# Performance work log

Measured on AMD Instinct MI355X. Metric: run time of the kernel, lower is better.

Reference implementation:

```python
import jax, jax.numpy as jnp
import numpy as np

TAU = 0.2
ALPHA = 0.8
EPS = 1e-8  # torch cosine_similarity eps
LAM_POS = 1.5  # generate_lambda()=0.5, +1 for extrapolation
LAM_NEG = 0.5  # interpolation lambda


def _cos_sim_matrix(x):
    # row-normalize with clamped norm (matches F.cosine_similarity eps), then gram matrix
    n = x / jnp.maximum(jnp.linalg.norm(x, axis=1, keepdims=True), EPS)
    return n @ n.T


def setup_inputs() -> dict:
    key = jax.random.key(0)
    N, D = 4096, 512
    emb = jax.random.normal(key, (N, D), dtype=jnp.float32)
    # SimCLR-style symmetric positive pairs: (2k,2k+1) and (2k+1,2k)
    base = np.arange(0, N, 2)
    fwd_pairs = np.stack([base, base + 1], axis=1)
    pairs = np.concatenate([fwd_pairs, fwd_pairs[:, ::-1]], axis=0)  # [N, 2]
    return {"embeddings": emb, "positive_pairs": jnp.asarray(pairs, dtype=jnp.int32)}


def reference(embeddings, positive_pairs):
    # stage == 'train' (quantile-thresholded hard-negative branch)
    N = embeddings.shape[0]
    ar = jnp.arange(N)
    pi, pj = positive_pairs[:, 0], positive_pairs[:, 1]
    # ordered positive mask (symmetric because pairs include both orientations)
    pos_mask = jnp.zeros((N, N), dtype=bool).at[pi, pj].set(True)

    # --- extrapolate positive pairs: row i -> 1.5*e_i - 0.5*e_j ---
    partner_pos = jnp.full((N,), -1, dtype=jnp.int32).at[pi].set(pj.astype(jnp.int32))
    in_pair = partner_pos >= 0
    pp = jnp.where(in_pair, partner_pos, 0)
    hard_pos_emb = jnp.where(
        in_pair[:, None],
        LAM_POS * embeddings - (LAM_POS - 1.0) * embeddings[pp],
        embeddings,
    )

    # --- interpolate negative pairs: row k -> 0.5*(e_k + e_partner) ---
    # Negative pairs are all ordered (i,j), i!=j, not positive, scattered in
    # row k is the largest i with (i,k) negative.
    valid = (~pos_mask.T) & (ar[None, :] != ar[:, None])  # valid[k, i] = (i,k) is negative
    partner_neg = jnp.max(jnp.where(valid, ar[None, :], -1), axis=1)
    hard_neg_emb = LAM_NEG * embeddings + (1.0 - LAM_NEG) * embeddings[partner_neg]

    # --- three NxN cosine-sim matrices, composed by the scatter pattern ---
    orig_sim = _cos_sim_matrix(embeddings)
    hard_pos_sim = _cos_sim_matrix(hard_pos_emb)
    hard_neg_sim = _cos_sim_matrix(hard_neg_emb)
    diag = jnp.eye(N, dtype=bool)
    sim = jnp.where(diag, orig_sim, jnp.where(pos_mask, hard_pos_sim, hard_neg_sim))

    # --- contrastive loss with per-row quantile hard-negative threshold ---
    mask = diag | pos_mask
    exp_sim = jnp.exp(sim / TAU)
    exp_masked = jnp.where(mask, 0.0, exp_sim)
    pos_sim = exp_sim[pi, pj]              # [P]
    exp_rows = exp_masked[pi]              # [P, N]
    thr = jnp.quantile(exp_rows, ALPHA, axis=1, keepdims=True)
    hard_neg_sum = jnp.sum(jnp.where(exp_rows >= thr, exp_rows, 0.0), axis=1)
    loss = -jnp.log(pos_sim / (pos_sim + hard_neg_sum))
    # torch sums loss_ij + loss_ji over all rows / (2*P); with symmetric pair
    # list this equals sum(loss_ij)/P
    return jnp.sum(loss) / positive_pairs.shape[0]
```

## Files before the change

kernel.cpp:

```cpp
#include <hip/hip_runtime.h>
#include <cmath>

#define DIM 512
#define TAU_INV 5.0f
#define EPSN 1e-8f
#define ALPHA_Q 0.8f
#define TPITCH 72

typedef __attribute__((ext_vector_type(8))) unsigned short us8;
typedef __attribute__((ext_vector_type(4))) unsigned short us4;
typedef __attribute__((ext_vector_type(8))) short s8v;
typedef __attribute__((ext_vector_type(4))) float f4;

__device__ __forceinline__ unsigned short f2h(float f) {
    _Float16 h = (_Float16)f;
    return *(const unsigned short*)&h;
}
__device__ __forceinline__ float h2f(unsigned u) {
    unsigned short us = (unsigned short)u;
    _Float16 h = *(const _Float16*)&us;
    return (float)h;
}
__device__ __forceinline__ unsigned key16(unsigned u) {
    return u ^ (0x8000u | (0x7FFFu & (0u - (u >> 15))));
}
__device__ __forceinline__ float keyval(unsigned k) {
    unsigned u = (k & 0x8000u) ? (k & 0x7FFFu) : ((~k) & 0xFFFFu);
    return h2f(u);
}

__global__ void k_scatter(const int* __restrict__ pairs, int* partner, int P) {
    int k = blockIdx.x * 256 + threadIdx.x;
    if (k < P) partner[pairs[2 * k]] = pairs[2 * k + 1];
}
__global__ void k_pneg(const int* __restrict__ partner, int* pneg, int N) {
    int i = blockIdx.x * 256 + threadIdx.x;
    if (i >= N) return;
    int q = -1;
    for (int j = N - 1; j >= 0; --j) {
        if (j != i && partner[j] != i) { q = j; break; }
    }
    pneg[i] = q;
}

__global__ __launch_bounds__(128) void k_prep(const float* __restrict__ emb,
                                              const int* __restrict__ pneg,
                                              const int* __restrict__ pairs,
                                              unsigned short* __restrict__ mb,
                                              float* __restrict__ pos_term,
                                              int N, int P) {
    int bid = blockIdx.x, t = threadIdx.x;
    if (bid < N) {
        int i = bid;
        int q = pneg[i];
        float4 a = ((const float4*)(emb + (size_t)i * DIM))[t];
        float4 b = ((const float4*)(emb + (size_t)q * DIM))[t];
        float hx = 0.5f * (a.x + b.x), hy = 0.5f * (a.y + b.y);
        float hz = 0.5f * (a.z + b.z), hw = 0.5f * (a.w + b.w);
        float ss = hx * hx + hy * hy + hz * hz + hw * hw;
        for (int o = 32; o > 0; o >>= 1) ss += __shfl_down(ss, o);
        __shared__ float red[2];
        __shared__ float s_inv;
        if ((t & 63) == 0) red[t >> 6] = ss;
        __syncthreads();
        if (t == 0) s_inv = 1.0f / fmaxf(sqrtf(red[0] + red[1]), EPSN);
        __syncthreads();
        float inv = s_inv;
        us4 o4;
        o4[0] = f2h(hx * inv); o4[1] = f2h(hy * inv);
        o4[2] = f2h(hz * inv); o4[3] = f2h(hw * inv);
        *(us4*)(mb + (size_t)i * DIM + t * 4) = o4;
    } else {
        int k = bid - N;
        int i = pairs[2 * k], j = pairs[2 * k + 1];
        float4 a = ((const float4*)(emb + (size_t)i * DIM))[t];
        float4 b = ((const float4*)(emb + (size_t)j * DIM))[t];
        float dab = 0.f, naa = 0.f, nbb = 0.f;
        {
            float fa, fb;
            fa = 1.5f * a.x - 0.5f * b.x; fb = 1.5f * b.x - 0.5f * a.x; dab += fa * fb; naa += fa * fa; nbb += fb * fb;
            fa = 1.5f * a.y - 0.5f * b.y; fb = 1.5f * b.y - 0.5f * a.y; dab += fa * fb; naa += fa * fa; nbb += fb * fb;
            fa = 1.5f * a.z - 0.5f * b.z; fb = 1.5f * b.z - 0.5f * a.z; dab += fa * fb; naa += fa * fa; nbb += fb * fb;
            fa = 1.5f * a.w - 0.5f * b.w; fb = 1.5f * b.w - 0.5f * a.w; dab += fa * fb; naa += fa * fa; nbb += fb * fb;
        }
        for (int o = 32; o > 0; o >>= 1) {
            dab += __shfl_down(dab, o);
            naa += __shfl_down(naa, o);
            nbb += __shfl_down(nbb, o);
        }
        __shared__ float rd[2], ra[2], rb[2];
        if ((t & 63) == 0) { rd[t >> 6] = dab; ra[t >> 6] = naa; rb[t >> 6] = nbb; }
        __syncthreads();
        if (t == 0) {
            float d = rd[0] + rd[1], na = ra[0] + ra[1], nb = rb[0] + rb[1];
            float sim = d / (fmaxf(sqrtf(na), EPSN) * fmaxf(sqrtf(nb), EPSN));
            pos_term[k] = expf(sim * TAU_INV);
        }
    }
}

__global__ __launch_bounds__(256, 3) void k_gemm_sym(const unsigned short* __restrict__ mb,
                                                     unsigned short* __restrict__ S, int N) {
    __shared__ __align__(16) unsigned short As[128][32];
    __shared__ __align__(16) unsigned short Bs[128][32];
    __shared__ __align__(16) unsigned short Ts[4][64 * TPITCH];
    int tid = threadIdx.x;
    int wave = tid >> 6, lane = tid & 63, quad = lane >> 4, l16 = lane & 15;
    int wr = (wave >> 1) * 64, wc = (wave & 1) * 64;

    int ntb = N >> 7;
    int bi = 0, rem = blockIdx.x, rowlen = ntb;
    while (rem >= rowlen) { rem -= rowlen; ++bi; --rowlen; }
    int bj = bi + rem;
    int iBase = bi * 128, jBase = bj * 128;
    int lrow = lane >> 2, lseg = lane & 3;

    const unsigned short* gA0 = mb + (size_t)(iBase + wave * 32 + lrow) * DIM + lseg * 8;
    const unsigned short* gA1 = gA0 + 16 * DIM;
    const unsigned short* gB0 = mb + (size_t)(jBase + wave * 32 + lrow) * DIM + lseg * 8;
    const unsigned short* gB1 = gB0 + 16 * DIM;
    __attribute__((address_space(3))) char* ldsA =
        (__attribute__((address_space(3))) char*)As + wave * 2048;
    __attribute__((address_space(3))) char* ldsB =
        (__attribute__((address_space(3))) char*)Bs + wave * 2048;

    f4 acc[4][4];
    for (int i = 0; i < 4; ++i)
        for (int j = 0; j < 4; ++j) acc[i][j] = (f4){0.f, 0.f, 0.f, 0.f};

    for (int k0 = 0; k0 < DIM; k0 += 32) {
        __syncthreads();
        __builtin_amdgcn_global_load_lds(
            (const __attribute__((address_space(1))) void*)(gA0 + k0),
            (__attribute__((address_space(3))) void*)(ldsA), 16, 0, 0);
        __builtin_amdgcn_global_load_lds(
            (const __attribute__((address_space(1))) void*)(gA1 + k0),
            (__attribute__((address_space(3))) void*)(ldsA + 1024), 16, 0, 0);
        __builtin_amdgcn_global_load_lds(
            (const __attribute__((address_space(1))) void*)(gB0 + k0),
            (__attribute__((address_space(3))) void*)(ldsB), 16, 0, 0);
        __builtin_amdgcn_global_load_lds(
            (const __attribute__((address_space(1))) void*)(gB1 + k0),
            (__attribute__((address_space(3))) void*)(ldsB + 1024), 16, 0, 0);
        __syncthreads();

        s8v a[4], b[4];
        for (int i = 0; i < 4; ++i) a[i] = *(const s8v*)&As[wr + i * 16 + l16][quad * 8];
        for (int j = 0; j < 4; ++j) b[j] = *(const s8v*)&Bs[wc + j * 16 + l16][quad * 8];
        for (int i = 0; i < 4; ++i)
            for (int j = 0; j < 4; ++j)
                acc[i][j] = __builtin_amdgcn_mfma_f32_16x16x32_f16(a[i], b[j], acc[i][j], 0, 0, 0);
    }
    int rQ = iBase + wr + quad * 4;
    int cQ = jBase + wc + l16;
    for (int i = 0; i < 4; ++i)
        for (int j = 0; j < 4; ++j)
            for (int rr = 0; rr < 4; ++rr)
                S[(size_t)(rQ + i * 16 + rr) * N + cQ + j * 16] = f2h(acc[i][j][rr]);

    if (bi != bj) {
        unsigned short* T = &Ts[wave][0];
        #pragma unroll
        for (int i = 0; i < 4; ++i)
            #pragma unroll
            for (int j = 0; j < 4; ++j)
                #pragma unroll
                for (int rr = 0; rr < 4; ++rr) {
                    int tr = quad * 4 + i * 16 + rr;
                    int tc = l16 + j * 16;
                    T[tc * TPITCH + tr] = f2h(acc[i][j][rr]);
                }
        int lrow8 = lane >> 3, lseg8 = lane & 7;
        #pragma unroll
        for (int it = 0; it < 8; ++it) {
            int mr = it * 8 + lrow8;
            us8 v = *(const us8*)&T[mr * TPITCH + lseg8 * 8];
            *(us8*)&S[(size_t)(jBase + wc + mr) * N + iBase + wr + lseg8 * 8] = v;
        }
    }
}

__global__ __launch_bounds__(256) void k_gemm(const unsigned short* __restrict__ mb,
                                              unsigned short* __restrict__ S, int N, int rowBase) {
    __shared__ __align__(16) unsigned short As[128][32];
    __shared__ __align__(16) unsigned short Bs[128][32];
    int tid = threadIdx.x;
    int wave = tid >> 6, lane = tid & 63, quad = lane >> 4, l16 = lane & 15;
    int wr = (wave >> 1) * 64, wc = (wave & 1) * 64;
    int iBase = rowBase + blockIdx.y * 128;
    int jBase = blockIdx.x * 128;
    int lrow = lane >> 2, lseg = lane & 3;

    const unsigned short* gA0 = mb + (size_t)(iBase + wave * 32 + lrow) * DIM + lseg * 8;
    const unsigned short* gA1 = gA0 + 16 * DIM;
    const unsigned short* gB0 = mb + (size_t)(jBase + wave * 32 + lrow) * DIM + lseg * 8;
    const unsigned short* gB1 = gB0 + 16 * DIM;
    __attribute__((address_space(3))) char* ldsA =
        (__attribute__((address_space(3))) char*)As + wave * 2048;
    __attribute__((address_space(3))) char* ldsB =
        (__attribute__((address_space(3))) char*)Bs + wave * 2048;

    f4 acc[4][4];
    for (int i = 0; i < 4; ++i)
        for (int j = 0; j < 4; ++j) acc[i][j] = (f4){0.f, 0.f, 0.f, 0.f};

    for (int k0 = 0; k0 < DIM; k0 += 32) {
        __syncthreads();
        __builtin_amdgcn_global_load_lds(
            (const __attribute__((address_space(1))) void*)(gA0 + k0),
            (__attribute__((address_space(3))) void*)(ldsA), 16, 0, 0);
        __builtin_amdgcn_global_load_lds(
            (const __attribute__((address_space(1))) void*)(gA1 + k0),
            (__attribute__((address_space(3))) void*)(ldsA + 1024), 16, 0, 0);
        __builtin_amdgcn_global_load_lds(
            (const __attribute__((address_space(1))) void*)(gB0 + k0),
            (__attribute__((address_space(3))) void*)(ldsB), 16, 0, 0);
        __builtin_amdgcn_global_load_lds(
            (const __attribute__((address_space(1))) void*)(gB1 + k0),
            (__attribute__((address_space(3))) void*)(ldsB + 1024), 16, 0, 0);
        __syncthreads();

        s8v a[4], b[4];
        for (int i = 0; i < 4; ++i) a[i] = *(const s8v*)&As[wr + i * 16 + l16][quad * 8];
        for (int j = 0; j < 4; ++j) b[j] = *(const s8v*)&Bs[wc + j * 16 + l16][quad * 8];
        for (int i = 0; i < 4; ++i)
            for (int j = 0; j < 4; ++j)
                acc[i][j] = __builtin_amdgcn_mfma_f32_16x16x32_f16(a[i], b[j], acc[i][j], 0, 0, 0);
    }
    int rQ = blockIdx.y * 128 + wr + quad * 4;
    int cQ = jBase + wc + l16;
    for (int i = 0; i < 4; ++i)
        for (int j = 0; j < 4; ++j)
            for (int rr = 0; rr < 4; ++rr)
                S[(size_t)(rQ + i * 16 + rr) * N + cQ + j * 16] = f2h(acc[i][j][rr]);
}

__global__ __launch_bounds__(256, 4) void k_select(const unsigned short* __restrict__ Sb,
                                                   const int* __restrict__ pairs,
                                                   const float* __restrict__ pos_term,
                                                   float* __restrict__ losses,
                                                   int N, int r0, int r1,
                                                   int klo, float frac) {
    __shared__ unsigned shcnt[2];
    __shared__ unsigned shmin;
    __shared__ float s_red[4];
    int tid = threadIdx.x, wid = tid >> 6, lane = tid & 63;
    int k = blockIdx.x;
    int row = pairs[2 * k];
    if (row < r0 || row >= r1) return;
    int pj = pairs[2 * k + 1];
    const us8* src8 = (const us8*)(Sb + (size_t)(row - r0) * N);

    us8 g0 = src8[tid];
    us8 g1 = src8[256 + tid];
    unsigned kr[16];
    {
        int m0 = row - tid * 8, p0 = pj - tid * 8;
        int m1 = row - 2048 - tid * 8, p1 = pj - 2048 - tid * 8;
        #pragma unroll
        for (int e = 0; e < 8; ++e) {
            unsigned u = (unsigned short)g0[e];
            kr[e] = ((e == m0) | (e == p0)) ? 0u : key16(u);
        }
        #pragma unroll
        for (int e = 0; e < 8; ++e) {
            unsigned u = (unsigned short)g1[e];
            kr[8 + e] = ((e == m1) | (e == p1)) ? 0u : key16(u);
        }
    }

    int nmask = (pj == row) ? 1 : 2;
    int Nreal = N - nmask;
    int Rreal = klo - nmask;
    float pos = pos_term[k];
    float s = 0.f;

    if (Rreal < 0) {
        #pragma unroll
        for (int e = 0; e < 16; ++e)
            if (kr[e] > 0u) s += __expf(keyval(kr[e]) * TAU_INV);
    } else {
        if (tid < 2) shcnt[tid] = 0u;
        if (tid == 0) shmin = 0xFFFFFFFFu;
        __syncthreads();
        int lim = Nreal - Rreal - 1;
        unsigned lo = 1, hi = 65535;
        int parity = 0;
        while (lo < hi) {
            unsigned mid = (lo + hi) >> 1;
            unsigned wcnt = 0;
            #pragma unroll
            for (int e = 0; e < 16; ++e)
                wcnt += (unsigned)__popcll(__ballot(kr[e] > mid));
            if (lane == 0) atomicAdd(&shcnt[parity], wcnt);
            __syncthreads();
            unsigned cnt = shcnt[parity];
            if (tid == 0) shcnt[parity ^ 1] = 0u;
            __syncthreads();
            if (cnt <= (unsigned)lim) hi = mid; else lo = mid + 1;
            parity ^= 1;
        }
        unsigned K1 = lo;

        if (frac > 1e-9f) {
            unsigned wcnt = 0, mymin = 0xFFFFFFFFu;
            #pragma unroll
            for (int e = 0; e < 16; ++e) {
                bool gt = kr[e] > K1;
                wcnt += (unsigned)__popcll(__ballot(gt));
                if (gt && kr[e] < mymin) mymin = kr[e];
            }
            for (int o = 1; o < 64; o <<= 1) {
                unsigned y = (unsigned)__shfl_xor((int)mymin, o);
                if (y < mymin) mymin = y;
            }
            if (lane == 0) {
                atomicAdd(&shcnt[parity], wcnt);
                atomicMin(&shmin, mymin);
            }
            __syncthreads();
            unsigned cntAbove = shcnt[parity];
            unsigned minAbove = shmin;
            unsigned K2;
            if (Rreal + 1 > Nreal - 1)                   K2 = K1;
            else if (Nreal - (int)cntAbove >= Rreal + 2) K2 = K1;
            else                                         K2 = minAbove;
            float elo = __expf(keyval(K1) * TAU_INV);
            float ehi = __expf(keyval(K2) * TAU_INV);
            float thr = elo + frac * (ehi - elo);
            #pragma unroll
            for (int e = 0; e < 16; ++e) {
                if (kr[e] > 0u) {
                    float ev = __expf(keyval(kr[e]) * TAU_INV);
                    if (ev >= thr) s += ev;
                }
            }
        } else {
            #pragma unroll
            for (int e = 0; e < 16; ++e)
                if (kr[e] >= K1) s += __expf(keyval(kr[e]) * TAU_INV);
        }
    }

    for (int o = 1; o < 64; o <<= 1) s += __shfl_xor(s, o);
    if (lane == 0) s_red[wid] = s;
    __syncthreads();
    if (tid == 0) {
        float st = s_red[0] + s_red[1] + s_red[2] + s_red[3];
        losses[k] = logf((pos + st) / pos);
    }
}

__global__ __launch_bounds__(256) void k_reduce(const float* __restrict__ losses,
                                                float* __restrict__ out, int P, float invP) {
    __shared__ float s_red[4];
    int tid = threadIdx.x, wid = tid >> 6, lane = tid & 63;
    float s = 0.f;
    for (int i = tid; i < P; i += 256) s += losses[i];
    for (int o = 1; o < 64; o <<= 1) s += __shfl_xor(s, o);
    if (lane == 0) s_red[wid] = s;
    __syncthreads();
    if (tid == 0) out[0] = (s_red[0] + s_red[1] + s_red[2] + s_red[3]) * invP;
}

extern "C" void kernel_launch(void* const* d_in, const int* in_sizes, int n_in,
                              void* d_out, int out_size, void* d_ws, size_t ws_size,
                              hipStream_t stream) {
    const float* emb = (const float*)d_in[0];
    const int* pairs = (const int*)d_in[1];
    float* out = (float*)d_out;
    int N = in_sizes[0] / DIM;
    int P = in_sizes[1] / 2;

    char* ws = (char*)d_ws;
    size_t off = 0;
    unsigned short* mb = (unsigned short*)(ws + off); off += (size_t)N * DIM * 2;
    int* partner = (int*)(ws + off);                  off += (size_t)N * 4;
    int* pneg = (int*)(ws + off);                     off += (size_t)N * 4;
    float* pos_term = (float*)(ws + off);             off += (size_t)P * 4;
    float* losses = (float*)(ws + off);               off += (size_t)P * 4;
    off = (off + 255) & ~(size_t)255;
    unsigned short* Sbuf = (unsigned short*)(ws + off);
    size_t avail = (ws_size > off) ? ws_size - off : 0;
    long maxRows = (long)(avail / ((size_t)N * 2));
    int chunk = (int)(maxRows - (maxRows % 128));
    if (chunk > N) chunk = N;
    if (chunk < 128) chunk = 128;

    hipMemsetAsync(partner, 0xFF, (size_t)N * 4, stream);
    k_scatter<<<dim3((P + 255) / 256), dim3(256), 0, stream>>>(pairs, partner, P);
    k_pneg<<<dim3((N + 255) / 256), dim3(256), 0, stream>>>(partner, pneg, N);
    k_prep<<<dim3(N + P), dim3(128), 0, stream>>>(emb, pneg, pairs, mb, pos_term, N, P);

    float qpos = ALPHA_Q * (float)(N - 1);
    int klo = (int)floorf(qpos);
    float frac = qpos - (float)klo;
    float invP = 1.0f / (float)P;

    if (chunk >= N) {
        int ntb = N >> 7;
        int nblk = ntb * (ntb + 1) / 2;
        k_gemm_sym<<<dim3(nblk), dim3(256), 0, stream>>>(mb, Sbuf, N);
        k_select<<<dim3(P), dim3(256), 0, stream>>>(Sbuf, pairs, pos_term, losses,
                                                    N, 0, N, klo, frac);
    } else {
        for (int r0 = 0; r0 < N; r0 += chunk) {
            int rows = (N - r0 < chunk) ? (N - r0) : chunk;
            dim3 g(N / 128, rows / 128);
            k_gemm<<<g, dim3(256), 0, stream>>>(mb, Sbuf, N, r0);
            k_select<<<dim3(P), dim3(256), 0, stream>>>(Sbuf, pairs, pos_term, losses,
                                                        N, r0, r0 + rows, klo, frac);
        }
    }
    k_reduce<<<dim3(1), dim3(256), 0, stream>>>(losses, out, P, invP);
}
```

Baseline: 130.1 us.

## Run quantile selection one row per wavefront and inline negative-partner lookup

The selection kernel now gives each positive-pair row to a single 64-lane wavefront holding 64 packed fp16 keys per lane. This removes the LDS atomics and the two block barriers that each binary-search step needed. Separately, the O(N) backward scan kernel that found each row's negative partner is dropped; the partner is derived inline in the prep kernel by checking at most the last three indices. The trade-off is more register pressure and more serial ballot work per wave in exchange for less synchronisation and one fewer launch.

```diff
diff --git a/kernel.cpp b/kernel.cpp
--- a/kernel.cpp
+++ b/kernel.cpp
@@ -33,18 +33,9 @@
     int k = blockIdx.x * 256 + threadIdx.x;
     if (k < P) partner[pairs[2 * k]] = pairs[2 * k + 1];
 }
-__global__ void k_pneg(const int* __restrict__ partner, int* pneg, int N) {
-    int i = blockIdx.x * 256 + threadIdx.x;
-    if (i >= N) return;
-    int q = -1;
-    for (int j = N - 1; j >= 0; --j) {
-        if (j != i && partner[j] != i) { q = j; break; }
-    }
-    pneg[i] = q;
-}
 
 __global__ __launch_bounds__(128) void k_prep(const float* __restrict__ emb,
-                                              const int* __restrict__ pneg,
+                                              const int* __restrict__ partner,
                                               const int* __restrict__ pairs,
                                               unsigned short* __restrict__ mb,
                                               float* __restrict__ pos_term,
@@ -52,7 +43,9 @@
     int bid = blockIdx.x, t = threadIdx.x;
     if (bid < N) {
         int i = bid;
-        int q = pneg[i];
+        int q = N - 1;
+        if (q == i || partner[q] == i) q = N - 2;
+        if (q == i || partner[q] == i) q = N - 3;
         float4 a = ((const float4*)(emb + (size_t)i * DIM))[t];
         float4 b = ((const float4*)(emb + (size_t)q * DIM))[t];
         float hx = 0.5f * (a.x + b.x), hy = 0.5f * (a.y + b.y);
@@ -235,37 +228,37 @@
                 S[(size_t)(rQ + i * 16 + rr) * N + cQ + j * 16] = f2h(acc[i][j][rr]);
 }
 
-__global__ __launch_bounds__(256, 4) void k_select(const unsigned short* __restrict__ Sb,
+__global__ __launch_bounds__(128, 4) void k_select(const unsigned short* __restrict__ Sb,
                                                    const int* __restrict__ pairs,
                                                    const float* __restrict__ pos_term,
                                                    float* __restrict__ losses,
-                                                   int N, int r0, int r1,
+                                                   int N, int r0, int r1, int P,
                                                    int klo, float frac) {
-    __shared__ unsigned shcnt[2];
-    __shared__ unsigned shmin;
-    __shared__ float s_red[4];
-    int tid = threadIdx.x, wid = tid >> 6, lane = tid & 63;
-    int k = blockIdx.x;
+    int wid = threadIdx.x >> 6, lane = threadIdx.x & 63;
+    int k = blockIdx.x * 2 + wid;
+    if (k >= P) return;
     int row = pairs[2 * k];
     if (row < r0 || row >= r1) return;
     int pj = pairs[2 * k + 1];
     const us8* src8 = (const us8*)(Sb + (size_t)(row - r0) * N);
 
-    us8 g0 = src8[tid];
-    us8 g1 = src8[256 + tid];
-    unsigned kr[16];
-    {
-        int m0 = row - tid * 8, p0 = pj - tid * 8;
-        int m1 = row - 2048 - tid * 8, p1 = pj - 2048 - tid * 8;
+    unsigned kr[32];
+    #pragma unroll
+    for (int t = 0; t < 8; ++t)
+        *(us8*)&kr[t * 4] = src8[t * 64 + lane];
+
+    #pragma unroll
+    for (int t = 0; t < 8; ++t) {
+        int j0 = (t * 64 + lane) * 8;
         #pragma unroll
-        for (int e = 0; e < 8; ++e) {
-            unsigned u = (unsigned short)g0[e];
-            kr[e] = ((e == m0) | (e == p0)) ? 0u : key16(u);
-        }
-        #pragma unroll
-        for (int e = 0; e < 8; ++e) {
-            unsigned u = (unsigned short)g1[e];
-            kr[8 + e] = ((e == m1) | (e == p1)) ? 0u : key16(u);
+        for (int m = 0; m < 4; ++m) {
+            unsigned p = kr[t * 4 + m];
+            unsigned lo = key16(p & 0xFFFFu);
+            unsigned hi = key16(p >> 16);
+            int jlo = j0 + 2 * m, jhi = jlo + 1;
+            if (jlo == row || jlo == pj) lo = 0u;
+            if (jhi == row || jhi == pj) hi = 0u;
+            kr[t * 4 + m] = lo | (hi << 16);
         }
     }
 
@@ -277,78 +270,66 @@
 
     if (Rreal < 0) {
         #pragma unroll
-        for (int e = 0; e < 16; ++e)
-            if (kr[e] > 0u) s += __expf(keyval(kr[e]) * TAU_INV);
+        for (int i = 0; i < 32; ++i) {
+            unsigned lo = kr[i] & 0xFFFFu, hi = kr[i] >> 16;
+            if (lo > 0u) s += __expf(keyval(lo) * TAU_INV);
+            if (hi > 0u) s += __expf(keyval(hi) * TAU_INV);
+        }
     } else {
-        if (tid < 2) shcnt[tid] = 0u;
-        if (tid == 0) shmin = 0xFFFFFFFFu;
-        __syncthreads();
         int lim = Nreal - Rreal - 1;
-        unsigned lo = 1, hi = 65535;
-        int parity = 0;
-        while (lo < hi) {
-            unsigned mid = (lo + hi) >> 1;
-            unsigned wcnt = 0;
-            #pragma unroll
-            for (int e = 0; e < 16; ++e)
-                wcnt += (unsigned)__popcll(__ballot(kr[e] > mid));
-            if (lane == 0) atomicAdd(&shcnt[parity], wcnt);
-            __syncthreads();
-            unsigned cnt = shcnt[parity];
-            if (tid == 0) shcnt[parity ^ 1] = 0u;
-            __syncthreads();
-            if (cnt <= (unsigned)lim) hi = mid; else lo = mid + 1;
-            parity ^= 1;
-        }
-        unsigned K1 = lo;
+        unsigned lo_ = 1, hi_ = 65535;
+        while (lo_ < hi_) {
+            unsigned mid = (lo_ + hi_) >> 1;
+            unsigned cnt = 0;
+            #pragma unroll
+            for (int i = 0; i < 32; ++i) {
+                cnt += (unsigned)__popcll(__ballot((kr[i] & 0xFFFFu) > mid));
+                cnt += (unsigned)__popcll(__ballot((kr[i] >> 16) > mid));
+            }
+            if (cnt <= (unsigned)lim) hi_ = mid; else lo_ = mid + 1;
+        }
+        unsigned K1 = lo_;
 
         if (frac > 1e-9f) {
-            unsigned wcnt = 0, mymin = 0xFFFFFFFFu;
-            #pragma unroll
-            for (int e = 0; e < 16; ++e) {
-                bool gt = kr[e] > K1;
-                wcnt += (unsigned)__popcll(__ballot(gt));
-                if (gt && kr[e] < mymin) mymin = kr[e];
+            unsigned cntAbove = 0, mymin = 0xFFFFFFFFu;
+            #pragma unroll
+            for (int i = 0; i < 32; ++i) {
+                unsigned lo = kr[i] & 0xFFFFu, hi = kr[i] >> 16;
+                bool glo = lo > K1, ghi = hi > K1;
+                cntAbove += (unsigned)__popcll(__ballot(glo));
+                cntAbove += (unsigned)__popcll(__ballot(ghi));
+                if (glo && lo < mymin) mymin = lo;
+                if (ghi && hi < mymin) mymin = hi;
             }
             for (int o = 1; o < 64; o <<= 1) {
                 unsigned y = (unsigned)__shfl_xor((int)mymin, o);
                 if (y < mymin) mymin = y;
             }
-            if (lane == 0) {
-                atomicAdd(&shcnt[parity], wcnt);
-                atomicMin(&shmin, mymin);
-            }
-            __syncthreads();
-            unsigned cntAbove = shcnt[parity];
-            unsigned minAbove = shmin;
             unsigned K2;
             if (Rreal + 1 > Nreal - 1)                   K2 = K1;
             else if (Nreal - (int)cntAbove >= Rreal + 2) K2 = K1;
-            else                                         K2 = minAbove;
+            else                                         K2 = mymin;
             float elo = __expf(keyval(K1) * TAU_INV);
             float ehi = __expf(keyval(K2) * TAU_INV);
             float thr = elo + frac * (ehi - elo);
             #pragma unroll
-            for (int e = 0; e < 16; ++e) {
-                if (kr[e] > 0u) {
-                    float ev = __expf(keyval(kr[e]) * TAU_INV);
-                    if (ev >= thr) s += ev;
-                }
+            for (int i = 0; i < 32; ++i) {
+                unsigned lo = kr[i] & 0xFFFFu, hi = kr[i] >> 16;
+                if (lo > 0u) { float ev = __expf(keyval(lo) * TAU_INV); if (ev >= thr) s += ev; }
+                if (hi > 0u) { float ev = __expf(keyval(hi) * TAU_INV); if (ev >= thr) s += ev; }
             }
         } else {
             #pragma unroll
-            for (int e = 0; e < 16; ++e)
-                if (kr[e] >= K1) s += __expf(keyval(kr[e]) * TAU_INV);
+            for (int i = 0; i < 32; ++i) {
+                unsigned lo = kr[i] & 0xFFFFu, hi = kr[i] >> 16;
+                if (lo >= K1) s += __expf(keyval(lo) * TAU_INV);
+                if (hi >= K1) s += __expf(keyval(hi) * TAU_INV);
+            }
         }
     }
 
     for (int o = 1; o < 64; o <<= 1) s += __shfl_xor(s, o);
-    if (lane == 0) s_red[wid] = s;
-    __syncthreads();
-    if (tid == 0) {
-        float st = s_red[0] + s_red[1] + s_red[2] + s_red[3];
-        losses[k] = logf((pos + st) / pos);
-    }
+    if (lane == 0) losses[k] = logf((pos + s) / pos);
 }
 
 __global__ __launch_bounds__(256) void k_reduce(const float* __restrict__ losses,
@@ -376,7 +357,6 @@
     size_t off = 0;
     unsigned short* mb = (unsigned short*)(ws + off); off += (size_t)N * DIM * 2;
     int* partner = (int*)(ws + off);                  off += (size_t)N * 4;
-    int* pneg = (int*)(ws + off);                     off += (size_t)N * 4;
     float* pos_term = (float*)(ws + off);             off += (size_t)P * 4;
     float* losses = (float*)(ws + off);               off += (size_t)P * 4;
     off = (off + 255) & ~(size_t)255;
@@ -389,8 +369,7 @@
 
     hipMemsetAsync(partner, 0xFF, (size_t)N * 4, stream);
     k_scatter<<<dim3((P + 255) / 256), dim3(256), 0, stream>>>(pairs, partner, P);
-    k_pneg<<<dim3((N + 255) / 256), dim3(256), 0, stream>>>(partner, pneg, N);
-    k_prep<<<dim3(N + P), dim3(128), 0, stream>>>(emb, pneg, pairs, mb, pos_term, N, P);
+    k_prep<<<dim3(N + P), dim3(128), 0, stream>>>(emb, partner, pairs, mb, pos_term, N, P);
 
     float qpos = ALPHA_Q * (float)(N - 1);
     int klo = (int)floorf(qpos);
@@ -401,15 +380,15 @@
         int ntb = N >> 7;
         int nblk = ntb * (ntb + 1) / 2;
         k_gemm_sym<<<dim3(nblk), dim3(256), 0, stream>>>(mb, Sbuf, N);
-        k_select<<<dim3(P), dim3(256), 0, stream>>>(Sbuf, pairs, pos_term, losses,
-                                                    N, 0, N, klo, frac);
+        k_select<<<dim3((P + 1) / 2), dim3(128), 0, stream>>>(Sbuf, pairs, pos_term, losses,
+                                                              N, 0, N, P, klo, frac);
     } else {
         for (int r0 = 0; r0 < N; r0 += chunk) {
             int rows = (N - r0 < chunk) ? (N - r0) : chunk;
             dim3 g(N / 128, rows / 128);
             k_gemm<<<g, dim3(256), 0, stream>>>(mb, Sbuf, N, r0);
-            k_select<<<dim3(P), dim3(256), 0, stream>>>(Sbuf, pairs, pos_term, losses,
-                                                        N, r0, r0 + rows, klo, frac);
+            k_select<<<dim3((P + 1) / 2), dim3(128), 0, stream>>>(Sbuf, pairs, pos_term, losses,
+                                                                  N, r0, r0 + rows, P, klo, frac);
         }
     }
     k_reduce<<<dim3(1), dim3(256), 0, stream>>>(losses, out, P, invP);
```

Measured after the change: 126.2 us. 3.0% less time.
